# Performance work log

Hardware: AMD Instinct MI355X
Metric: run time of the kernel (lower is better)

## Reference

```python
import jax, jax.numpy as jnp
import numpy as np

B, C, H = 16, 512, 32
HID, NB, S, P, SR = 512, 36, 26, 7, 2
SCALE = 32.0
N_LOC, N_LOC_LAB = 12, 8
N_GRP, GRP_SZ, N_GRP_LAB = 4, 6, 16
IN_DIM = P * P * C


def roi_align(feat, coords, scale, pooled, sr):
    # feat: (B,C,H,W); coords: (B,NB,4) normalized xyxy. torchvision roi_align,
    # aligned=False, fixed sampling_ratio=sr (adaptive ratio is data-dependent).
    Bs, Cc, Hh, Ww = feat.shape
    x1 = coords[..., 0] * scale
    y1 = coords[..., 1] * scale
    x2 = coords[..., 2] * scale
    y2 = coords[..., 3] * scale
    rw = jnp.maximum(x2 - x1, 1.0)
    rh = jnp.maximum(y2 - y1, 1.0)
    bw = rw / pooled
    bh = rh / pooled
    # sample offsets within roi, in bin units: (pooled*sr,)
    off = (jnp.arange(pooled)[:, None] + (jnp.arange(sr) + 0.5) / sr).reshape(-1)
    ys = y1[..., None] + off * bh[..., None]  # (B,NB,pooled*sr)
    xs = x1[..., None] + off * bw[..., None]

    def prep(t, size):
        valid = (t > -1.0) & (t < size)
        tc = jnp.clip(t, 0.0, size - 1)
        lo = jnp.floor(tc).astype(jnp.int32)
        hi = jnp.minimum(lo + 1, size - 1)
        frac = tc - lo
        return lo, hi, frac, valid

    y_lo, y_hi, ly, vy = prep(ys, Hh)
    x_lo, x_hi, lx, vx = prep(xs, Ww)
    hy, hx = 1.0 - ly, 1.0 - lx

    featl = feat.transpose(0, 2, 3, 1)  # (B,H,W,C)
    b_idx = jnp.arange(Bs)[:, None, None, None]

    def gather(yi, xi):
        # -> (B,NB,Py,Px,C)
        return featl[b_idx, yi[:, :, :, None], xi[:, :, None, :]]

    def w(a, b):
        return (a[..., :, None] * b[..., None, :])[..., None]

    val = (gather(y_lo, x_lo) * w(hy, hx) + gather(y_lo, x_hi) * w(hy, lx)
           + gather(y_hi, x_lo) * w(ly, hx) + gather(y_hi, x_hi) * w(ly, lx))
    mask = (vy[:, :, :, None] & vx[:, :, None, :])[..., None]
    val = jnp.where(mask, val, 0.0)
    val = val.reshape(Bs, -1, pooled, sr, pooled, sr, Cc).mean(axis=(3, 5))
    return val.transpose(0, 1, 4, 2, 3)  # (B,NB,C,pooled,pooled)


def setup_inputs() -> dict:
    key = jax.random.key(0)
    ks = jax.random.split(key, 10)
    lf = jax.random.normal(ks[0], (B, C, H, H), dtype=jnp.float32)
    xs = jnp.sort(jax.random.uniform(ks[1], (B, S, 2)), axis=-1)
    ys = jnp.sort(jax.random.uniform(ks[2], (B, S, 2)), axis=-1)
    coords = jnp.stack([xs[..., 0], ys[..., 0], xs[..., 1], ys[..., 1]], axis=-1)
    sc = 0.02
    return {
        'local_features': lf,
        'pred_bbox_coords': coords,
        'roi_fc_W': jax.random.normal(ks[3], (HID, IN_DIM), dtype=jnp.float32) * sc,
        'roi_fc_b': jnp.zeros((HID,), jnp.float32),
        'coords_W': jax.random.normal(ks[4], (S, 4, HID), dtype=jnp.float32) * sc,
        'coords_b': jnp.zeros((S, 4), jnp.float32),
        'pres_W': jax.random.normal(ks[5], (S, HID), dtype=jnp.float32) * sc,
        'pres_b': jnp.zeros((S,), jnp.float32),
        'loc_W': jax.random.normal(ks[6], (N_LOC, N_LOC_LAB, HID), dtype=jnp.float32) * sc,
        'loc_b': jnp.zeros((N_LOC, N_LOC_LAB), jnp.float32),
        'grp_W': jax.random.normal(ks[7], (N_GRP, N_GRP_LAB, GRP_SZ * HID), dtype=jnp.float32) * sc,
        'grp_b': jnp.zeros((N_GRP, N_GRP_LAB), jnp.float32),
        'loc_idx': jnp.arange(N_LOC, dtype=jnp.int32),
        'grp_idx': jnp.arange(N_GRP * GRP_SZ, dtype=jnp.int32).reshape(N_GRP, GRP_SZ),
    }


def reference(local_features, pred_bbox_coords, roi_fc_W, roi_fc_b, coords_W,
              coords_b, pres_W, pres_b, loc_W, loc_b, grp_W, grp_b, loc_idx, grp_idx):
    Bs = local_features.shape[0]
    # boxes S..NB default to the full image (0,0,1,1)
    full = jnp.broadcast_to(jnp.array([0.0, 0.0, 1.0, 1.0], jnp.float32), (Bs, NB, 4))
    coords_all = full.at[:, :S].set(pred_bbox_coords)
    roi = roi_align(local_features, coords_all, SCALE, P, SR)  # (B,NB,C,P,P)
    flat = roi.reshape(Bs, NB, IN_DIM)
    feats = jax.nn.relu(jnp.einsum('bnf,hf->bnh', flat, roi_fc_W) + roi_fc_b)
    sup = feats[:, :S]  # (B,S,HID)
    # per-box coord refinement heads
    deltas = jnp.einsum('bsh,soh->bso', sup, coords_W) + coords_b  # (B,S,4)
    w = pred_bbox_coords[..., 2] - pred_bbox_coords[..., 0]
    h = pred_bbox_coords[..., 3] - pred_bbox_coords[..., 1]
    wh = jnp.stack([w, h, w, h], axis=-1)
    refined = pred_bbox_coords + deltas * wh
    presence = jnp.einsum('bsh,sh->bs', sup, pres_W) + pres_b  # (B,S)
    # per-box MLC heads
    loc = jnp.einsum('blh,loh->blo', feats[:, loc_idx], loc_W) + loc_b
    # per-group MLC heads (concat box feats within group along hidden)
    gf = feats[:, grp_idx].reshape(Bs, N_GRP, GRP_SZ * HID)
    grp = jnp.einsum('bgk,gok->bgo', gf, grp_W) + grp_b
    mlc = jnp.concatenate([loc.reshape(Bs, -1), grp.reshape(Bs, -1)], axis=1)
    return refined, presence, mlc
```

## Files before the change

kernel.cpp:

```cpp
#include <hip/hip_runtime.h>

typedef unsigned short u16;
typedef __attribute__((ext_vector_type(8))) short short8;
typedef __attribute__((ext_vector_type(8))) unsigned short ushort8_t;
typedef __attribute__((ext_vector_type(4))) float f32x4;
typedef __attribute__((ext_vector_type(2))) float v2f;

#define BATCH   16
#define CCH     512
#define NBOX    36
#define SS      26
#define INDIM   25088
#define HIDN    512
#define M_ROWS  576
#define KSPLIT  28
#define KITERS  14
#define NKB     392

__device__ __forceinline__ u16 f2bf(float f) {
  unsigned u = __float_as_uint(f);
  u += 0x7FFF + ((u >> 16) & 1);
  return (u16)(u >> 16);
}
__device__ __forceinline__ float bf2f(u16 h) {
  return __uint_as_float(((unsigned)h) << 16);
}
__device__ __forceinline__ v2f bf2x2(u16 a, u16 b) {
  v2f r;
  r.x = __uint_as_float(((unsigned)a) << 16);
  r.y = __uint_as_float(((unsigned)b) << 16);
  return r;
}

__global__ __launch_bounds__(256) void k_transpose_lf(const float* __restrict__ in,
                                                      u16* __restrict__ out) {
  __shared__ u16 t[32][66];
  int b = blockIdx.z, y = blockIdx.y, ct = blockIdx.x;
  int tid = threadIdx.x;

  int cl = tid >> 2;
  int xq = (tid & 3) * 8;
  const float* src = in + ((size_t)(b * CCH + ct * 64 + cl) * 1024) + y * 32 + xq;
  float4 v0 = *(const float4*)src;
  float4 v1 = *(const float4*)(src + 4);
  t[xq + 0][cl] = f2bf(v0.x); t[xq + 1][cl] = f2bf(v0.y);
  t[xq + 2][cl] = f2bf(v0.z); t[xq + 3][cl] = f2bf(v0.w);
  t[xq + 4][cl] = f2bf(v1.x); t[xq + 5][cl] = f2bf(v1.y);
  t[xq + 6][cl] = f2bf(v1.z); t[xq + 7][cl] = f2bf(v1.w);
  __syncthreads();

  int xl = tid >> 3;
  int cq = (tid & 7) * 8;
  ushort8_t o;
#pragma unroll
  for (int i = 0; i < 8; ++i) o[i] = t[xl][cq + i];
  *(ushort8_t*)(out + ((size_t)b * 1024 + y * 32 + xl) * CCH + ct * 64 + cq) = o;
}

#define WPAD 532
__global__ __launch_bounds__(256) void k_convert_w(const float* __restrict__ in,
                                                   u16* __restrict__ out) {
  __shared__ u16 s[49 * WPAD];
  int h = blockIdx.x;
  int tid = threadIdx.x;
  const float4* src = (const float4*)(in + (size_t)h * INDIM);
  for (int i = tid; i < 6272; i += 256) {
    float4 v = src[i];
    int k = i * 4;
#pragma unroll
    for (int j = 0; j < 4; ++j) {
      int kk = k + j;
      int c = kk / 49;
      int p = kk - c * 49;
      s[p * WPAD + c] = f2bf((&v.x)[j]);
    }
  }
  __syncthreads();
  for (int q = tid; q < 3136; q += 256) {
    int p = q >> 6;
    int c0 = (q & 63) * 8;
    const u16* sp = &s[p * WPAD + c0];
    ushort8_t o;
#pragma unroll
    for (int i = 0; i < 8; ++i) o[i] = sp[i];
    int kb = p * 8 + (c0 >> 6);
    int col = c0 & 63;
    *(ushort8_t*)(out + ((size_t)kb * HIDN + h) * 64 + col) = o;
  }
}

__global__ __launch_bounds__(512) void k_roi(const u16* __restrict__ lf_t,
                                             const float* __restrict__ pred,
                                             u16* __restrict__ flat2) {
  __shared__ int   s_ylo[14], s_yhi[14], s_xlo[14], s_xhi[14];
  __shared__ float s_wyl[14], s_wyh[14], s_wxl[14], s_wxh[14];

  int blk = blockIdx.x;
  int b = blk / NBOX, n = blk % NBOX;
  int t = threadIdx.x;

  if (t < 28) {
    bool isY = t < 14;
    int j = isY ? t : t - 14;
    float c0, c1, c2, c3;
    if (n < SS) {
      const float* p = pred + ((size_t)(b * SS + n)) * 4;
      c0 = p[0]; c1 = p[1]; c2 = p[2]; c3 = p[3];
    } else { c0 = 0.f; c1 = 0.f; c2 = 1.f; c3 = 1.f; }
    float lo1 = (isY ? c1 : c0) * 32.f;
    float hi1 = (isY ? c3 : c2) * 32.f;
    float sz = fmaxf(hi1 - lo1, 1.f);
    float bs = sz * (1.f / 7.f);
    float off = (float)(j >> 1) + 0.25f + 0.5f * (float)(j & 1);
    float pos = lo1 + off * bs;
    bool valid = (pos > -1.f) && (pos < 32.f);
    float tc = fminf(fmaxf(pos, 0.f), 31.f);
    int lo = (int)floorf(tc);
    int hi = min(lo + 1, 31);
    float fr = tc - (float)lo;
    float wl = valid ? (1.f - fr) : 0.f;
    float wh = valid ? fr : 0.f;
    if (isY) { s_ylo[j] = lo; s_yhi[j] = hi; s_wyl[j] = wl; s_wyh[j] = wh; }
    else     { s_xlo[j] = lo; s_xhi[j] = hi; s_wxl[j] = wl; s_wxh[j] = wh; }
  }
  __syncthreads();

  int cg = t & 63;
  int pg = t >> 6;
  const u16* base = lf_t + (size_t)b * 1024 * CCH + cg * 8;

  for (int p = pg; p < 49; p += 8) {
    int py = p / 7, px = p % 7;
    v2f a0 = {0.f, 0.f}, a1 = {0.f, 0.f}, a2 = {0.f, 0.f}, a3 = {0.f, 0.f};
#pragma unroll
    for (int sy = 0; sy < 2; ++sy) {
      int jy = 2 * py + sy;
      const u16* rlo = base + s_ylo[jy] * 32 * CCH;
      const u16* rhi = base + s_yhi[jy] * 32 * CCH;
      float wyl = s_wyl[jy], wyh = s_wyh[jy];
#pragma unroll
      for (int sx = 0; sx < 2; ++sx) {
        int jx = 2 * px + sx;
        int xl = s_xlo[jx] * CCH, xh = s_xhi[jx] * CCH;
        v2f wll = {wyl * s_wxl[jx], wyl * s_wxl[jx]};
        v2f wlh = {wyl * s_wxh[jx], wyl * s_wxh[jx]};
        v2f whl = {wyh * s_wxl[jx], wyh * s_wxl[jx]};
        v2f whh = {wyh * s_wxh[jx], wyh * s_wxh[jx]};
        ushort8_t vll = *(const ushort8_t*)(rlo + xl);
        ushort8_t vlh = *(const ushort8_t*)(rlo + xh);
        ushort8_t vhl = *(const ushort8_t*)(rhi + xl);
        ushort8_t vhh = *(const ushort8_t*)(rhi + xh);
        a0 += wll * bf2x2(vll[0], vll[1]) + wlh * bf2x2(vlh[0], vlh[1])
            + whl * bf2x2(vhl[0], vhl[1]) + whh * bf2x2(vhh[0], vhh[1]);
        a1 += wll * bf2x2(vll[2], vll[3]) + wlh * bf2x2(vlh[2], vlh[3])
            + whl * bf2x2(vhl[2], vhl[3]) + whh * bf2x2(vhh[2], vhh[3]);
        a2 += wll * bf2x2(vll[4], vll[5]) + wlh * bf2x2(vlh[4], vlh[5])
            + whl * bf2x2(vhl[4], vhl[5]) + whh * bf2x2(vhh[4], vhh[5]);
        a3 += wll * bf2x2(vll[6], vll[7]) + wlh * bf2x2(vlh[6], vlh[7])
            + whl * bf2x2(vhl[6], vhl[7]) + whh * bf2x2(vhh[6], vhh[7]);
      }
    }
    ushort8_t o;
    o[0] = f2bf(a0.x * 0.25f); o[1] = f2bf(a0.y * 0.25f);
    o[2] = f2bf(a1.x * 0.25f); o[3] = f2bf(a1.y * 0.25f);
    o[4] = f2bf(a2.x * 0.25f); o[5] = f2bf(a2.y * 0.25f);
    o[6] = f2bf(a3.x * 0.25f); o[7] = f2bf(a3.y * 0.25f);
    int kb = p * 8 + (cg >> 3);
    int col = (cg & 7) * 8;
    *(ushort8_t*)(flat2 + ((size_t)kb * M_ROWS + blk) * 64 + col) = o;
  }
}

__global__ __launch_bounds__(256) void k_gemm(const u16* __restrict__ flat2,
                                              const u16* __restrict__ Wb2,
                                              float* __restrict__ partials) {
  __shared__ u16 As[128 * 64];
  __shared__ u16 Bs[128 * 64];

  int tid = threadIdx.x;
  int wave = tid >> 6, lane = tid & 63;
  int wm = wave >> 1, wn = wave & 1;
  int quad = lane >> 4, r = lane & 15;
  int xb = r & 7;

  int tileM0 = blockIdx.y * 128;
  int tileN0 = blockIdx.x * 128;
  int kb0 = blockIdx.z * KITERS;

  size_t aoff[4], boff[4];
  int    ldso[4];
#pragma unroll
  for (int t = 0; t < 4; ++t) {
    int chunk = (wave * 4 + t) * 64 + lane;
    int row = chunk >> 3;
    int lc = chunk & 7;
    ldso[t] = row * 64 + ((lc ^ (row & 7)) << 3);
    int grow = min(tileM0 + row, M_ROWS - 1);
    aoff[t] = ((size_t)kb0 * M_ROWS + grow) * 64 + lc * 8;
    boff[t] = ((size_t)kb0 * HIDN + tileN0 + row) * 64 + lc * 8;
  }

  f32x4 acc[4][4];
#pragma unroll
  for (int mi = 0; mi < 4; ++mi)
#pragma unroll
    for (int ni = 0; ni < 4; ++ni) acc[mi][ni] = (f32x4){0.f, 0.f, 0.f, 0.f};

  short8 ra[4], rb[4];
#pragma unroll
  for (int t = 0; t < 4; ++t) {
    ra[t] = *(const short8*)(flat2 + aoff[t]);
    rb[t] = *(const short8*)(Wb2 + boff[t]);
  }

  for (int kt = 0; kt < KITERS; ++kt) {
#pragma unroll
    for (int t = 0; t < 4; ++t) {
      *(short8*)&As[ldso[t]] = ra[t];
      *(short8*)&Bs[ldso[t]] = rb[t];
    }
    __syncthreads();

    if (kt + 1 < KITERS) {
      size_t ak = (size_t)(kt + 1) * (M_ROWS * 64);
      size_t bk = (size_t)(kt + 1) * (HIDN * 64);
#pragma unroll
      for (int t = 0; t < 4; ++t) {
        ra[t] = *(const short8*)(flat2 + aoff[t] + ak);
        rb[t] = *(const short8*)(Wb2 + boff[t] + bk);
      }
    }

#pragma unroll
    for (int kk = 0; kk < 64; kk += 32) {
      int k8 = kk >> 3;
      int pc = ((k8 + quad) ^ xb) << 3;
      short8 af[4], bfr[4];
#pragma unroll
      for (int mi = 0; mi < 4; ++mi)
        af[mi] = *(const short8*)&As[(wm * 64 + mi * 16 + r) * 64 + pc];
#pragma unroll
      for (int ni = 0; ni < 4; ++ni)
        bfr[ni] = *(const short8*)&Bs[(wn * 64 + ni * 16 + r) * 64 + pc];
#pragma unroll
      for (int mi = 0; mi < 4; ++mi)
#pragma unroll
        for (int ni = 0; ni < 4; ++ni)
          acc[mi][ni] = __builtin_amdgcn_mfma_f32_16x16x32_bf16(
              af[mi], bfr[ni], acc[mi][ni], 0, 0, 0);
    }
    __syncthreads();
  }

  float* part = partials + (size_t)blockIdx.z * (M_ROWS * HIDN);
#pragma unroll
  for (int mi = 0; mi < 4; ++mi)
#pragma unroll
    for (int ni = 0; ni < 4; ++ni) {
      int row0 = tileM0 + wm * 64 + mi * 16 + quad * 4;
      int col = tileN0 + wn * 64 + ni * 16 + r;
#pragma unroll
      for (int reg = 0; reg < 4; ++reg) {
        int row = row0 + reg;
        if (row < M_ROWS) part[(size_t)row * HIDN + col] = acc[mi][ni][reg];
      }
    }
}

__global__ __launch_bounds__(256) void k_reduce(const float4* __restrict__ partials,
                                                const float* __restrict__ bias,
                                                float4* __restrict__ feats) {
  int gid = blockIdx.x * 256 + threadIdx.x;
  int h4 = gid & (HIDN / 4 - 1);
  float4 s = {0.f, 0.f, 0.f, 0.f};
#pragma unroll
  for (int k = 0; k < KSPLIT; ++k) {
    float4 v = partials[(size_t)k * (M_ROWS * HIDN / 4) + gid];
    s.x += v.x; s.y += v.y; s.z += v.z; s.w += v.w;
  }
  const float* bi = bias + h4 * 4;
  s.x = fmaxf(s.x + bi[0], 0.f);
  s.y = fmaxf(s.y + bi[1], 0.f);
  s.z = fmaxf(s.z + bi[2], 0.f);
  s.w = fmaxf(s.w + bi[3], 0.f);
  feats[gid] = s;
}

__device__ __forceinline__ float wave_red(float s) {
#pragma unroll
  for (int off = 32; off > 0; off >>= 1) s += __shfl_down(s, off);
  return s;
}

__device__ __forceinline__ float dot512(const float* __restrict__ f,
                                        const float* __restrict__ w, int lane) {
  const float4* f4 = (const float4*)f;
  const float4* w4 = (const float4*)w;
  float4 x0 = f4[lane], y0 = w4[lane];
  float4 x1 = f4[lane + 64], y1 = w4[lane + 64];
  return x0.x * y0.x + x0.y * y0.y + x0.z * y0.z + x0.w * y0.w +
         x1.x * y1.x + x1.y * y1.y + x1.z * y1.z + x1.w * y1.w;
}

__global__ __launch_bounds__(256) void k_heads(const float* __restrict__ feats,
                                               const float* __restrict__ pred,
                                               const float* __restrict__ cW,
                                               const float* __restrict__ cb,
                                               const float* __restrict__ pW,
                                               const float* __restrict__ pb,
                                               const float* __restrict__ lW,
                                               const float* __restrict__ lb,
                                               const float* __restrict__ gW,
                                               const float* __restrict__ gb,
                                               const int* __restrict__ lidx,
                                               const int* __restrict__ gidx,
                                               float* __restrict__ out) {
  int wid = blockIdx.x * 4 + (threadIdx.x >> 6);
  int lane = threadIdx.x & 63;
  float sum = 0.f;

  if (wid < 1664) {
    int b = wid / 104, rr = wid % 104, s = rr >> 2, o = rr & 3;
    sum = dot512(feats + (size_t)(b * NBOX + s) * HIDN,
                 cW + (size_t)(s * 4 + o) * HIDN, lane);
    sum = wave_red(sum);
    if (lane == 0) {
      const float* p = pred + (size_t)(b * SS + s) * 4;
      float wdt = p[2] - p[0], hgt = p[3] - p[1];
      float whv = (o & 1) ? hgt : wdt;
      out[wid] = p[o] + (sum + cb[s * 4 + o]) * whv;
    }
  } else if (wid < 2080) {
    int i = wid - 1664;
    int b = i / 26, s = i % 26;
    sum = dot512(feats + (size_t)(b * NBOX + s) * HIDN,
                 pW + (size_t)s * HIDN, lane);
    sum = wave_red(sum);
    if (lane == 0) out[1664 + i] = sum + pb[s];
  } else if (wid < 3616) {
    int i = wid - 2080;
    int b = i / 96, rr = i % 96, l = rr >> 3, o = rr & 7;
    sum = dot512(feats + (size_t)(b * NBOX + lidx[l]) * HIDN,
                 lW + (size_t)(l * 8 + o) * HIDN, lane);
    sum = wave_red(sum);
    if (lane == 0) out[2080 + b * 160 + rr] = sum + lb[l * 8 + o];
  } else {
    int i = wid - 3616;
    int b = i / 64, rr = i % 64, g = rr >> 4, o = rr & 15;
    const float* w = gW + (size_t)(g * 16 + o) * 3072;
#pragma unroll
    for (int jj = 0; jj < 6; ++jj) {
      sum += dot512(feats + (size_t)(b * NBOX + gidx[g * 6 + jj]) * HIDN,
                    w + jj * 512, lane);
    }
    sum = wave_red(sum);
    if (lane == 0) out[2080 + b * 160 + 96 + rr] = sum + gb[g * 16 + o];
  }
}

extern "C" void kernel_launch(void* const* d_in, const int* in_sizes, int n_in,
                              void* d_out, int out_size, void* d_ws, size_t ws_size,
                              hipStream_t stream) {
  const float* lf      = (const float*)d_in[0];
  const float* pred    = (const float*)d_in[1];
  const float* roiW    = (const float*)d_in[2];
  const float* roiB    = (const float*)d_in[3];
  const float* cW      = (const float*)d_in[4];
  const float* cb      = (const float*)d_in[5];
  const float* pW      = (const float*)d_in[6];
  const float* pb      = (const float*)d_in[7];
  const float* lW      = (const float*)d_in[8];
  const float* lb      = (const float*)d_in[9];
  const float* gW      = (const float*)d_in[10];
  const float* gb      = (const float*)d_in[11];
  const int*   lidx    = (const int*)d_in[12];
  const int*   gidx    = (const int*)d_in[13];
  float* out = (float*)d_out;

  char* ws = (char*)d_ws;
  u16*   lf_t     = (u16*)ws;
  float* partials = (float*)ws;
  u16*   Wb2   = (u16*)(ws + 33030144);
  u16*   flat2 = (u16*)(ws + 33030144 + 25690112);
  float* feats = (float*)(ws + 33030144 + 25690112 + 28901376);

  k_transpose_lf<<<dim3(8, 32, 16), 256, 0, stream>>>(lf, lf_t);
  k_convert_w<<<HIDN, 256, 0, stream>>>(roiW, Wb2);
  k_roi<<<576, 512, 0, stream>>>(lf_t, pred, flat2);
  k_gemm<<<dim3(4, 5, KSPLIT), 256, 0, stream>>>(flat2, Wb2, partials);
  k_reduce<<<(M_ROWS * HIDN / 4) / 256, 256, 0, stream>>>(
      (const float4*)partials, roiB, (float4*)feats);
  k_heads<<<1160, 256, 0, stream>>>(feats, pred, cW, cb, pW, pb, lW, lb, gW, gb,
                                    lidx, gidx, out);
}
```

Baseline: 231.9 us.

## Drop LDS staging in split-K GEMM, load MFMA fragments directly from global

The GEMM no longer stages A/B tiles through shared memory with barriers. Each wave now loads its MFMA fragments straight from the pre-blocked global layout. Tiles become 64 rows by 256 columns per block (64x64 per wave), and the grid changes to 2x9x28 so that the 576 rows tile exactly, which removes the row bounds check. This removes LDS writes and reads and the syncthreads, but gives up sharing A across waves, so global/L2 traffic for A goes up and the register-prefetch pipelining is lost.

```diff
diff --git a/kernel.cpp b/kernel.cpp
--- a/kernel.cpp
+++ b/kernel.cpp
@@ -174,82 +174,46 @@
 __global__ __launch_bounds__(256) void k_gemm(const u16* __restrict__ flat2,
                                               const u16* __restrict__ Wb2,
                                               float* __restrict__ partials) {
-  __shared__ u16 As[128 * 64];
-  __shared__ u16 Bs[128 * 64];
-
   int tid = threadIdx.x;
   int wave = tid >> 6, lane = tid & 63;
-  int wm = wave >> 1, wn = wave & 1;
   int quad = lane >> 4, r = lane & 15;
-  int xb = r & 7;
-
-  int tileM0 = blockIdx.y * 128;
-  int tileN0 = blockIdx.x * 128;
+
+  int m0 = blockIdx.y * 64;
+  int n0 = (blockIdx.x * 4 + wave) * 64;
   int kb0 = blockIdx.z * KITERS;
 
-  size_t aoff[4], boff[4];
-  int    ldso[4];
-#pragma unroll
-  for (int t = 0; t < 4; ++t) {
-    int chunk = (wave * 4 + t) * 64 + lane;
-    int row = chunk >> 3;
-    int lc = chunk & 7;
-    ldso[t] = row * 64 + ((lc ^ (row & 7)) << 3);
-    int grow = min(tileM0 + row, M_ROWS - 1);
-    aoff[t] = ((size_t)kb0 * M_ROWS + grow) * 64 + lc * 8;
-    boff[t] = ((size_t)kb0 * HIDN + tileN0 + row) * 64 + lc * 8;
-  }
-
   f32x4 acc[4][4];
 #pragma unroll
   for (int mi = 0; mi < 4; ++mi)
 #pragma unroll
     for (int ni = 0; ni < 4; ++ni) acc[mi][ni] = (f32x4){0.f, 0.f, 0.f, 0.f};
 
-  short8 ra[4], rb[4];
-#pragma unroll
-  for (int t = 0; t < 4; ++t) {
-    ra[t] = *(const short8*)(flat2 + aoff[t]);
-    rb[t] = *(const short8*)(Wb2 + boff[t]);
-  }
-
+  const u16* aB = flat2 + ((size_t)kb0 * M_ROWS + m0 + r) * 64 + quad * 8;
+  const u16* bB = Wb2  + ((size_t)kb0 * HIDN  + n0 + r) * 64 + quad * 8;
+
+#pragma unroll 2
   for (int kt = 0; kt < KITERS; ++kt) {
-#pragma unroll
-    for (int t = 0; t < 4; ++t) {
-      *(short8*)&As[ldso[t]] = ra[t];
-      *(short8*)&Bs[ldso[t]] = rb[t];
-    }
-    __syncthreads();
-
-    if (kt + 1 < KITERS) {
-      size_t ak = (size_t)(kt + 1) * (M_ROWS * 64);
-      size_t bk = (size_t)(kt + 1) * (HIDN * 64);
-#pragma unroll
-      for (int t = 0; t < 4; ++t) {
-        ra[t] = *(const short8*)(flat2 + aoff[t] + ak);
-        rb[t] = *(const short8*)(Wb2 + boff[t] + bk);
-      }
-    }
-
-#pragma unroll
-    for (int kk = 0; kk < 64; kk += 32) {
-      int k8 = kk >> 3;
-      int pc = ((k8 + quad) ^ xb) << 3;
-      short8 af[4], bfr[4];
-#pragma unroll
-      for (int mi = 0; mi < 4; ++mi)
-        af[mi] = *(const short8*)&As[(wm * 64 + mi * 16 + r) * 64 + pc];
-#pragma unroll
-      for (int ni = 0; ni < 4; ++ni)
-        bfr[ni] = *(const short8*)&Bs[(wn * 64 + ni * 16 + r) * 64 + pc];
+    const u16* a = aB + (size_t)kt * (M_ROWS * 64);
+    const u16* b = bB + (size_t)kt * (HIDN * 64);
+    short8 af[2][4], bfr[2][4];
+#pragma unroll
+    for (int mi = 0; mi < 4; ++mi) {
+      af[0][mi] = *(const short8*)(a + mi * 1024);
+      af[1][mi] = *(const short8*)(a + mi * 1024 + 32);
+    }
+#pragma unroll
+    for (int ni = 0; ni < 4; ++ni) {
+      bfr[0][ni] = *(const short8*)(b + ni * 1024);
+      bfr[1][ni] = *(const short8*)(b + ni * 1024 + 32);
+    }
+#pragma unroll
+    for (int kk = 0; kk < 2; ++kk)
 #pragma unroll
       for (int mi = 0; mi < 4; ++mi)
 #pragma unroll
         for (int ni = 0; ni < 4; ++ni)
           acc[mi][ni] = __builtin_amdgcn_mfma_f32_16x16x32_bf16(
-              af[mi], bfr[ni], acc[mi][ni], 0, 0, 0);
-    }
-    __syncthreads();
+              af[kk][mi], bfr[kk][ni], acc[mi][ni], 0, 0, 0);
   }
 
   float* part = partials + (size_t)blockIdx.z * (M_ROWS * HIDN);
@@ -257,13 +221,11 @@
   for (int mi = 0; mi < 4; ++mi)
 #pragma unroll
     for (int ni = 0; ni < 4; ++ni) {
-      int row0 = tileM0 + wm * 64 + mi * 16 + quad * 4;
-      int col = tileN0 + wn * 64 + ni * 16 + r;
-#pragma unroll
-      for (int reg = 0; reg < 4; ++reg) {
-        int row = row0 + reg;
-        if (row < M_ROWS) part[(size_t)row * HIDN + col] = acc[mi][ni][reg];
-      }
+      int row0 = m0 + mi * 16 + quad * 4;
+      int col = n0 + ni * 16 + r;
+#pragma unroll
+      for (int reg = 0; reg < 4; ++reg)
+        part[(size_t)(row0 + reg) * HIDN + col] = acc[mi][ni][reg];
     }
 }
 
@@ -387,7 +349,7 @@
   k_transpose_lf<<<dim3(8, 32, 16), 256, 0, stream>>>(lf, lf_t);
   k_convert_w<<<HIDN, 256, 0, stream>>>(roiW, Wb2);
   k_roi<<<576, 512, 0, stream>>>(lf_t, pred, flat2);
-  k_gemm<<<dim3(4, 5, KSPLIT), 256, 0, stream>>>(flat2, Wb2, partials);
+  k_gemm<<<dim3(2, 9, KSPLIT), 256, 0, stream>>>(flat2, Wb2, partials);
   k_reduce<<<(M_ROWS * HIDN / 4) / 256, 256, 0, stream>>>(
       (const float4*)partials, roiB, (float4*)feats);
   k_heads<<<1160, 256, 0, stream>>>(feats, pred, cW, cb, pW, pb, lW, lb, gW, gb,
```

Measured after the change: 244.7 us. +5.5%, slower.

## Double split-K, store bf16 partials, and remap blocks for XCD locality

Applied to the files above, without the earlier changes.

Doubles the split-K factor so the GEMM launches 1120 blocks with half the K iterations each, and flattens the grid with an XCD-aware block-to-tile mapping. The same mapping in the ROI kernel keeps each batch's boxes on one XCD. Split-K partials are now written as bf16 instead of fp32, which halves partial traffic per split, and the reduce kernel reads 8 bf16 values per thread. The aim is better CU occupancy and cache locality, in exchange for more partials to reduce and a loss of precision from rounding the partials to bf16.

```diff
diff --git a/kernel.cpp b/kernel.cpp
--- a/kernel.cpp
+++ b/kernel.cpp
@@ -13,8 +13,8 @@
 #define INDIM   25088
 #define HIDN    512
 #define M_ROWS  576
-#define KSPLIT  28
-#define KITERS  14
+#define KSPLIT  56
+#define KITERS  7
 #define NKB     392
 
 __device__ __forceinline__ u16 f2bf(float f) {
@@ -95,8 +95,12 @@
   __shared__ int   s_ylo[14], s_yhi[14], s_xlo[14], s_xhi[14];
   __shared__ float s_wyl[14], s_wyh[14], s_wxl[14], s_wxh[14];
 
-  int blk = blockIdx.x;
-  int b = blk / NBOX, n = blk % NBOX;
+  int bid = blockIdx.x;
+  int xcd = bid & 7;
+  int s = bid >> 3;
+  int b = xcd * 2 + (s >= 36 ? 1 : 0);
+  int n = (s >= 36) ? s - 36 : s;
+  int blk = b * NBOX + n;
   int t = threadIdx.x;
 
   if (t < 28) {
@@ -173,7 +177,7 @@
 
 __global__ __launch_bounds__(256) void k_gemm(const u16* __restrict__ flat2,
                                               const u16* __restrict__ Wb2,
-                                              float* __restrict__ partials) {
+                                              u16* __restrict__ partials) {
   __shared__ u16 As[128 * 64];
   __shared__ u16 Bs[128 * 64];
 
@@ -183,9 +187,14 @@
   int quad = lane >> 4, r = lane & 15;
   int xb = r & 7;
 
-  int tileM0 = blockIdx.y * 128;
-  int tileN0 = blockIdx.x * 128;
-  int kb0 = blockIdx.z * KITERS;
+  int bid = blockIdx.x;
+  int xcd = bid & 7;
+  int slot = bid >> 3;
+  int z = xcd * 7 + slot / 20;
+  int xy = slot % 20;
+  int tileN0 = (xy & 3) * 128;
+  int tileM0 = (xy >> 2) * 128;
+  int kb0 = z * KITERS;
 
   size_t aoff[4], boff[4];
   int    ldso[4];
@@ -252,7 +261,7 @@
     __syncthreads();
   }
 
-  float* part = partials + (size_t)blockIdx.z * (M_ROWS * HIDN);
+  u16* part = partials + (size_t)z * (M_ROWS * HIDN);
 #pragma unroll
   for (int mi = 0; mi < 4; ++mi)
 #pragma unroll
@@ -262,28 +271,33 @@
 #pragma unroll
       for (int reg = 0; reg < 4; ++reg) {
         int row = row0 + reg;
-        if (row < M_ROWS) part[(size_t)row * HIDN + col] = acc[mi][ni][reg];
+        if (row < M_ROWS) part[(size_t)row * HIDN + col] = f2bf(acc[mi][ni][reg]);
       }
     }
 }
 
-__global__ __launch_bounds__(256) void k_reduce(const float4* __restrict__ partials,
+__global__ __launch_bounds__(256) void k_reduce(const u16* __restrict__ partials,
                                                 const float* __restrict__ bias,
-                                                float4* __restrict__ feats) {
+                                                float* __restrict__ feats) {
   int gid = blockIdx.x * 256 + threadIdx.x;
-  int h4 = gid & (HIDN / 4 - 1);
-  float4 s = {0.f, 0.f, 0.f, 0.f};
-#pragma unroll
-  for (int k = 0; k < KSPLIT; ++k) {
-    float4 v = partials[(size_t)k * (M_ROWS * HIDN / 4) + gid];
-    s.x += v.x; s.y += v.y; s.z += v.z; s.w += v.w;
-  }
-  const float* bi = bias + h4 * 4;
-  s.x = fmaxf(s.x + bi[0], 0.f);
-  s.y = fmaxf(s.y + bi[1], 0.f);
-  s.z = fmaxf(s.z + bi[2], 0.f);
-  s.w = fmaxf(s.w + bi[3], 0.f);
-  feats[gid] = s;
+  int row = gid >> 6;
+  int c0 = (gid & 63) * 8;
+  float s[8] = {0.f, 0.f, 0.f, 0.f, 0.f, 0.f, 0.f, 0.f};
+  const u16* p = partials + (size_t)row * HIDN + c0;
+  for (int z = 0; z < KSPLIT; ++z) {
+    ushort8_t v = *(const ushort8_t*)(p + (size_t)z * (M_ROWS * HIDN));
+#pragma unroll
+    for (int j = 0; j < 8; ++j) s[j] += bf2f(v[j]);
+  }
+  float4 o0, o1;
+  const float* bi = bias + c0;
+  o0.x = fmaxf(s[0] + bi[0], 0.f); o0.y = fmaxf(s[1] + bi[1], 0.f);
+  o0.z = fmaxf(s[2] + bi[2], 0.f); o0.w = fmaxf(s[3] + bi[3], 0.f);
+  o1.x = fmaxf(s[4] + bi[4], 0.f); o1.y = fmaxf(s[5] + bi[5], 0.f);
+  o1.z = fmaxf(s[6] + bi[6], 0.f); o1.w = fmaxf(s[7] + bi[7], 0.f);
+  float* dst = feats + (size_t)row * HIDN + c0;
+  *(float4*)dst = o0;
+  *(float4*)(dst + 4) = o1;
 }
 
 __device__ __forceinline__ float wave_red(float s) {
@@ -379,7 +393,7 @@
 
   char* ws = (char*)d_ws;
   u16*   lf_t     = (u16*)ws;
-  float* partials = (float*)ws;
+  u16*   partials = (u16*)ws;
   u16*   Wb2   = (u16*)(ws + 33030144);
   u16*   flat2 = (u16*)(ws + 33030144 + 25690112);
   float* feats = (float*)(ws + 33030144 + 25690112 + 28901376);
@@ -387,9 +401,8 @@
   k_transpose_lf<<<dim3(8, 32, 16), 256, 0, stream>>>(lf, lf_t);
   k_convert_w<<<HIDN, 256, 0, stream>>>(roiW, Wb2);
   k_roi<<<576, 512, 0, stream>>>(lf_t, pred, flat2);
-  k_gemm<<<dim3(4, 5, KSPLIT), 256, 0, stream>>>(flat2, Wb2, partials);
-  k_reduce<<<(M_ROWS * HIDN / 4) / 256, 256, 0, stream>>>(
-      (const float4*)partials, roiB, (float4*)feats);
+  k_gemm<<<1120, 256, 0, stream>>>(flat2, Wb2, partials);
+  k_reduce<<<(M_ROWS * HIDN / 8) / 256, 256, 0, stream>>>(partials, roiB, feats);
   k_heads<<<1160, 256, 0, stream>>>(feats, pred, cW, cb, pW, pb, lW, lb, gW, gb,
                                     lidx, gidx, out);
 }
```

New measurement: 217.9 us. -6.0%, faster.
